# Performance work log

Measured on AMD Instinct MI355X. Metric: run time of the kernel, lower is better.

The kernel has to match this reference:

```python
import jax, jax.numpy as jnp
import numpy as np
from jax import lax

K = 5  # carafe kernel size


def conv2d(x, w, b=None, padding='SAME'):
    y = lax.conv_general_dilated(x, w, (1, 1), padding,
                                 dimension_numbers=('NHWC', 'HWIO', 'NHWC'))
    return y if b is None else y + b


def upsample2x(x):
    return jnp.repeat(jnp.repeat(x, 2, axis=1), 2, axis=2)


def carafe(coarse, kernel):
    # coarse: [B,H,W,C]; kernel: [B,2H,2W,K*K] predicted at fine resolution
    B, H, W, C = coarse.shape
    pad = K // 2
    p = jnp.pad(coarse, ((0, 0), (pad, pad), (pad, pad), (0, 0)))
    # [B,H,W,K*K,C] neighborhoods, row-major (di,dj) order
    patches = jnp.stack([p[:, di:di + H, dj:dj + W, :]
                         for di in range(K) for dj in range(K)], axis=3)
    # softmax-normalized reassembly weights; fine pixel (i,j) -> coarse (i//2,j//2)
    mask = jax.nn.softmax(kernel, axis=-1).reshape(B, H, 2, W, 2, K * K)
    out = jnp.einsum('bhxwyk,bhwkc->bhxwyc', mask, patches)
    return out.reshape(B, 2 * H, 2 * W, C)


def setup_inputs() -> dict:
    key = jax.random.key(0)
    ks = jax.random.split(key, 8)
    B, H, W = 4, 64, 64
    Cf, Cc, E, F = 128, 256, 64, 256
    s = lambda k, shape: jax.random.normal(k, shape, jnp.float32) * 0.05
    z = lambda n: jnp.zeros((n,), jnp.float32)
    return dict(
        fine=jax.random.normal(ks[0], (B, 2 * H, 2 * W, Cf), jnp.float32),
        coarse=jax.random.normal(ks[1], (B, H, W, Cc), jnp.float32),
        gate_w=s(ks[2], (1, 1, Cc, 1)), gate_b=z(1),
        ss_fine_w=s(ks[3], (1, 1, Cf, E)), ss_fine_b=z(E),
        ss_coarse_w=s(ks[4], (1, 1, Cc, E)),
        ss_content_w=s(ks[5], (3, 3, E, K * K)), ss_content_b=z(K * K),
        coarse_proj_w=s(ks[6], (1, 1, Cc, F)), coarse_proj_b=z(F),
        fine_proj_w=s(ks[7], (1, 1, F, F)), fine_proj_b=z(F),
    )


def reference(fine, coarse, gate_w, gate_b, ss_fine_w, ss_fine_b, ss_coarse_w,
              ss_content_w, ss_content_b, coarse_proj_w, coarse_proj_b,
              fine_proj_w, fine_proj_b):
    # gate branch: 1x1 conv + sigmoid on coarse, nearest-upsample to fine size
    gate = upsample2x(jax.nn.sigmoid(conv2d(coarse, gate_w, gate_b)))
    # SemiShift kernel prediction: shared 3x3 'content' conv on both embeddings
    f = conv2d(conv2d(fine, ss_fine_w, ss_fine_b), ss_content_w, ss_content_b)
    c = conv2d(conv2d(coarse, ss_coarse_w), ss_content_w, ss_content_b)
    kernel = f + upsample2x(c)  # [B,2H,2W,K*K]
    # CARAFE content-aware reassembly of coarse at fine resolution
    cu = carafe(coarse, kernel)
    c_out = conv2d(cu, coarse_proj_w, coarse_proj_b)
    # NOTE: faithful to source -- 'fine' projection is applied to the coarse output
    f_out = conv2d(c_out, fine_proj_w, fine_proj_b)
    return gate * f_out + (1.0 - gate) * c_out
```

## Files before the change

### kernel.cpp

```cpp
#include <hip/hip_runtime.h>
#include <math.h>

constexpr int Bb = 4, Hc = 64, Wc = 64, Cc = 256, Cf = 128, E = 64, KK = 25, F = 256;
constexpr int Hf = 128, Wf = 128;
constexpr int Nc = Bb * Hc * Wc;
constexpr int Nf = Bb * Hf * Wf;

typedef __attribute__((ext_vector_type(8))) short bf16x8;
typedef __attribute__((ext_vector_type(4))) float f32x4;

__device__ inline unsigned short f2b(float f) {
  union { float f; unsigned u; } v; v.f = f;
  return (unsigned short)((v.u + 0x7FFF + ((v.u >> 16) & 1)) >> 16);
}

__global__ __launch_bounds__(256) void prepA_kernel(
    const float* __restrict__ fw, const float* __restrict__ cw,
    const float* __restrict__ cntw, unsigned short* __restrict__ Wtf,
    unsigned short* __restrict__ Wtc, unsigned short* __restrict__ Wtcnt) {
  int gid = blockIdx.x * 256 + threadIdx.x;
  if (gid < 8192) {
    int i = gid;
    int n = i & 63, k = i >> 6;
    Wtf[n * 128 + k] = f2b(fw[i]);
  } else if (gid < 8192 + 16384) {
    int i = gid - 8192;
    int n = i & 63, k = i >> 6;
    Wtc[n * 256 + k] = f2b(cw[i]);
  } else if (gid < 8192 + 16384 + 18432) {
    int i = gid - 8192 - 16384;
    int n = i & 31, kk = i >> 5;
    Wtcnt[n * 576 + kk] = (n < 25) ? f2b(cntw[kk * 25 + n]) : (unsigned short)0;
  }
}

template <int K>
__device__ inline void emb_body(const float* __restrict__ in,
                                const unsigned short* __restrict__ Wt,
                                const float* __restrict__ bias,
                                unsigned short* __restrict__ out, int pxb,
                                unsigned short* a_s ) {
  constexpr int LDA = 136;
  int t = threadIdx.x;
  int wid = t >> 6, lane = t & 63;
  int lr = lane & 15, lg = lane >> 4;
  const f32x4 zero4 = {0.f, 0.f, 0.f, 0.f};
  f32x4 acc[4] = {zero4, zero4, zero4, zero4};

  #pragma unroll
  for (int c0 = 0; c0 < K; c0 += 128) {
    for (int idx = t; idx < 64 * 32; idx += 256) {
      int px = idx >> 5, kc = idx & 31;
      float4 v = *(const float4*)&in[(size_t)(pxb + px) * K + c0 + kc * 4];
      *(short4*)&a_s[px * LDA + kc * 4] =
          make_short4((short)f2b(v.x), (short)f2b(v.y), (short)f2b(v.z), (short)f2b(v.w));
    }
    __syncthreads();
    #pragma unroll
    for (int kt = 0; kt < 4; kt++) {
      bf16x8 a = *(const bf16x8*)&a_s[(wid * 16 + lr) * LDA + kt * 32 + lg * 8];
      #pragma unroll
      for (int nt = 0; nt < 4; nt++) {
        bf16x8 bb = *(const bf16x8*)&Wt[(size_t)(nt * 16 + lr) * K + c0 + kt * 32 + lg * 8];
        acc[nt] = __builtin_amdgcn_mfma_f32_16x16x32_bf16(a, bb, acc[nt], 0, 0, 0);
      }
    }
    if (c0 + 128 < K) __syncthreads();
  }

  #pragma unroll
  for (int nt = 0; nt < 4; nt++) {
    int n = nt * 16 + lr;
    float bv = bias ? bias[n] : 0.f;
    #pragma unroll
    for (int r = 0; r < 4; r++) {
      int px = wid * 16 + lg * 4 + r;
      out[(size_t)(pxb + px) * 64 + n] = f2b(acc[nt][r] + bv);
    }
  }
}

__global__ __launch_bounds__(256) void emb_both_kernel(
    const float* __restrict__ fine, const unsigned short* __restrict__ Wtf,
    const float* __restrict__ fbias, unsigned short* __restrict__ femb,
    const float* __restrict__ coarse, const unsigned short* __restrict__ Wtc,
    unsigned short* __restrict__ cemb) {
  __shared__ __align__(16) unsigned short a_s[64 * 136];
  int idx = blockIdx.x;
  if (idx < Nf / 64) emb_body<128>(fine, Wtf, fbias, femb, idx * 64, a_s);
  else               emb_body<256>(coarse, Wtc, nullptr, cemb, (idx - Nf / 64) * 64, a_s);
}

__global__ __launch_bounds__(256) void content_fused_kernel(
    const unsigned short* __restrict__ femb, const unsigned short* __restrict__ cemb,
    const unsigned short* __restrict__ Wtcnt, const float* __restrict__ cb,
    float* __restrict__ kff, float* __restrict__ kfc,
    const float* __restrict__ coarse, const float* __restrict__ gw,
    const float* __restrict__ gb, float* __restrict__ gatec,
    const float* __restrict__ W1, const float* __restrict__ W2,
    unsigned short* __restrict__ Wt1, unsigned short* __restrict__ Wt12,
    float* __restrict__ b12f, const float* __restrict__ b1,
    const float* __restrict__ b2) {
  __shared__ __align__(16) unsigned short a_s[324 * 72];
  int idx = blockIdx.x, t = threadIdx.x;

  if (idx < 256) {
    int w = t >> 6, lane = t & 63;
    int base = idx * 64 + w * 16;
    const float4 wv = *(const float4*)(gw + lane * 4);
    float gb0 = gb[0];
    #pragma unroll
    for (int rnd = 0; rnd < 2; rnd++) {
      int p0 = base + rnd * 8;
      float a0, a1, a2, a3, a4, a5, a6, a7;
      {
        float4 v0 = *(const float4*)(coarse + (size_t)(p0 + 0) * 256 + lane * 4);
        float4 v1 = *(const float4*)(coarse + (size_t)(p0 + 1) * 256 + lane * 4);
        float4 v2 = *(const float4*)(coarse + (size_t)(p0 + 2) * 256 + lane * 4);
        float4 v3 = *(const float4*)(coarse + (size_t)(p0 + 3) * 256 + lane * 4);
        float4 v4 = *(const float4*)(coarse + (size_t)(p0 + 4) * 256 + lane * 4);
        float4 v5 = *(const float4*)(coarse + (size_t)(p0 + 5) * 256 + lane * 4);
        float4 v6 = *(const float4*)(coarse + (size_t)(p0 + 6) * 256 + lane * 4);
        float4 v7 = *(const float4*)(coarse + (size_t)(p0 + 7) * 256 + lane * 4);
        a0 = v0.x * wv.x + v0.y * wv.y + v0.z * wv.z + v0.w * wv.w;
        a1 = v1.x * wv.x + v1.y * wv.y + v1.z * wv.z + v1.w * wv.w;
        a2 = v2.x * wv.x + v2.y * wv.y + v2.z * wv.z + v2.w * wv.w;
        a3 = v3.x * wv.x + v3.y * wv.y + v3.z * wv.z + v3.w * wv.w;
        a4 = v4.x * wv.x + v4.y * wv.y + v4.z * wv.z + v4.w * wv.w;
        a5 = v5.x * wv.x + v5.y * wv.y + v5.z * wv.z + v5.w * wv.w;
        a6 = v6.x * wv.x + v6.y * wv.y + v6.z * wv.z + v6.w * wv.w;
        a7 = v7.x * wv.x + v7.y * wv.y + v7.z * wv.z + v7.w * wv.w;
      }
      #pragma unroll
      for (int off2 = 32; off2; off2 >>= 1) {
        a0 += __shfl_xor(a0, off2);
        a1 += __shfl_xor(a1, off2);
        a2 += __shfl_xor(a2, off2);
        a3 += __shfl_xor(a3, off2);
        a4 += __shfl_xor(a4, off2);
        a5 += __shfl_xor(a5, off2);
        a6 += __shfl_xor(a6, off2);
        a7 += __shfl_xor(a7, off2);
      }
      if (lane == 0) {
        gatec[p0 + 0] = 1.f / (1.f + expf(-(a0 + gb0)));
        gatec[p0 + 1] = 1.f / (1.f + expf(-(a1 + gb0)));
        gatec[p0 + 2] = 1.f / (1.f + expf(-(a2 + gb0)));
        gatec[p0 + 3] = 1.f / (1.f + expf(-(a3 + gb0)));
        gatec[p0 + 4] = 1.f / (1.f + expf(-(a4 + gb0)));
        gatec[p0 + 5] = 1.f / (1.f + expf(-(a5 + gb0)));
        gatec[p0 + 6] = 1.f / (1.f + expf(-(a6 + gb0)));
        gatec[p0 + 7] = 1.f / (1.f + expf(-(a7 + gb0)));
      }
    }
    return;
  } else if (idx < 272) {
    float (*tile)[65] = (float(*)[65])a_s;
    int sub = idx - 256;
    int k0 = ((sub >> 2) & 3) * 64, n0 = (sub & 3) * 64;
    int r0 = t >> 6, c = t & 63;
    #pragma unroll
    for (int r = r0; r < 64; r += 4)
      tile[r][c] = W1[(size_t)(k0 + r) * 256 + n0 + c];
    __syncthreads();
    #pragma unroll
    for (int r = r0; r < 64; r += 4)
      Wt1[(size_t)(n0 + r) * 256 + k0 + c] = f2b(tile[c][r]);
    return;
  } else if (idx < 288) {
    unsigned short* aa = a_s;
    unsigned short* bs = a_s + 64 * 72;
    int sub = idx - 272;
    int nbase = (sub & 3) * 64, k0 = (sub >> 2) * 64;
    int wid = t >> 6, lane = t & 63;
    int lr = lane & 15, lg = lane >> 4;
    const f32x4 zero4 = {0.f, 0.f, 0.f, 0.f};
    f32x4 acc[4] = {zero4, zero4, zero4, zero4};

    for (int mc = 0; mc < 4; mc++) {
      for (int i = t; i < 64 * 16; i += 256) {
        int r = i >> 4, c4 = i & 15;
        float4 v = *(const float4*)&W1[(size_t)(k0 + r) * 256 + mc * 64 + c4 * 4];
        *(short4*)&aa[r * 72 + c4 * 4] =
            make_short4((short)f2b(v.x), (short)f2b(v.y), (short)f2b(v.z), (short)f2b(v.w));
      }
      for (int i = t; i < 64 * 16; i += 256) {
        int m = i >> 4, n4 = i & 15;
        float4 v = *(const float4*)&W2[(size_t)(mc * 64 + m) * 256 + nbase + n4 * 4];
        bs[(n4 * 4 + 0) * 72 + m] = f2b(v.x);
        bs[(n4 * 4 + 1) * 72 + m] = f2b(v.y);
        bs[(n4 * 4 + 2) * 72 + m] = f2b(v.z);
        bs[(n4 * 4 + 3) * 72 + m] = f2b(v.w);
      }
      __syncthreads();
      #pragma unroll
      for (int kt = 0; kt < 2; kt++) {
        bf16x8 a = *(const bf16x8*)&aa[(wid * 16 + lr) * 72 + kt * 32 + lg * 8];
        #pragma unroll
        for (int nt = 0; nt < 4; nt++) {
          bf16x8 bb = *(const bf16x8*)&bs[(nt * 16 + lr) * 72 + kt * 32 + lg * 8];
          acc[nt] = __builtin_amdgcn_mfma_f32_16x16x32_bf16(a, bb, acc[nt], 0, 0, 0);
        }
      }
      __syncthreads();
    }
    #pragma unroll
    for (int nt = 0; nt < 4; nt++)
      #pragma unroll
      for (int r = 0; r < 4; r++)
        Wt12[(size_t)(nbase + nt * 16 + lr) * 256 + k0 + wid * 16 + lg * 4 + r] =
            f2b(acc[nt][r]);
    return;
  } else if (idx == 288) {
    int n = t;
    float a0 = 0.f, a1 = 0.f, a2 = 0.f, a3 = 0.f;
    #pragma unroll 4
    for (int m = 0; m < 256; m += 4) {
      a0 += b1[m + 0] * W2[(size_t)(m + 0) * 256 + n];
      a1 += b1[m + 1] * W2[(size_t)(m + 1) * 256 + n];
      a2 += b1[m + 2] * W2[(size_t)(m + 2) * 256 + n];
      a3 += b1[m + 3] * W2[(size_t)(m + 3) * 256 + n];
    }
    b12f[n] = (a0 + a1) + (a2 + a3) + b2[n];
    return;
  }

  int cidx = idx - 289;
  const unsigned short* emb;
  float* out;
  int b, i0, j0, Hd, Wd;
  if (cidx < 256) {
    b = cidx >> 6; int rem = cidx & 63;
    i0 = (rem >> 3) * 16; j0 = (rem & 7) * 16; Hd = 128; Wd = 128;
    emb = femb; out = kff;
  } else {
    int i2 = cidx - 256;
    b = i2 >> 4; int rem = i2 & 15;
    i0 = (rem >> 2) * 16; j0 = (rem & 3) * 16; Hd = 64; Wd = 64;
    emb = cemb; out = kfc;
  }

  for (int i = t; i < 324 * 16; i += 256) {
    int cell = i >> 4, ck = i & 15;
    int gi = i0 - 1 + cell / 18;
    int gj = j0 - 1 + cell % 18;
    short4 v = make_short4(0, 0, 0, 0);
    if (gi >= 0 && gi < Hd && gj >= 0 && gj < Wd)
      v = *(const short4*)&emb[(size_t)((b * Hd + gi) * Wd + gj) * 64 + ck * 4];
    *(short4*)&a_s[cell * 72 + ck * 4] = v;
  }
  __syncthreads();

  int wid = t >> 6, lane = t & 63;
  int lr = lane & 15, lg = lane >> 4;
  const f32x4 zero4 = {0.f, 0.f, 0.f, 0.f};
  f32x4 acc[4][2];
  #pragma unroll
  for (int mt = 0; mt < 4; mt++)
    #pragma unroll
    for (int nt = 0; nt < 2; nt++) acc[mt][nt] = zero4;

  #pragma unroll
  for (int nt = 0; nt < 2; nt++) {
    bf16x8 wb[9][2];
    #pragma unroll
    for (int tap = 0; tap < 9; tap++)
      #pragma unroll
      for (int kt = 0; kt < 2; kt++)
        wb[tap][kt] = *(const bf16x8*)&Wtcnt[(size_t)(nt * 16 + lr) * 576 + tap * 64 + kt * 32 + lg * 8];

    #pragma unroll
    for (int mt = 0; mt < 4; mt++) {
      int m = wid * 4 + mt;
      #pragma unroll
      for (int di = 0; di < 3; di++) {
        #pragma unroll
        for (int dj = 0; dj < 3; dj++) {
          int cell = (m + di) * 18 + (lr + dj);
          int tap = di * 3 + dj;
          #pragma unroll
          for (int kt = 0; kt < 2; kt++) {
            bf16x8 a = *(const bf16x8*)&a_s[cell * 72 + kt * 32 + lg * 8];
            acc[mt][nt] = __builtin_amdgcn_mfma_f32_16x16x32_bf16(a, wb[tap][kt], acc[mt][nt], 0, 0, 0);
          }
        }
      }
    }
  }

  #pragma unroll
  for (int mt = 0; mt < 4; mt++) {
    int m = wid * 4 + mt;
    int gi = i0 + m;
    #pragma unroll
    for (int nt = 0; nt < 2; nt++) {
      int ch = nt * 16 + lr;
      if (ch < 25) {
        float bv = cb[ch];
        #pragma unroll
        for (int r = 0; r < 4; r++) {
          int gj = j0 + lg * 4 + r;
          out[(size_t)((b * Hd + gi) * Wd + gj) * 25 + ch] = acc[mt][nt][r] + bv;
        }
      }
    }
  }
}

__global__ __launch_bounds__(256) void carafe_kernel(
    const float* __restrict__ coarse, const float* __restrict__ kff,
    const float* __restrict__ kfc, unsigned short* __restrict__ cu_g) {
  __shared__ __align__(16) unsigned short buf[256 * 72];
  __shared__ __align__(16) unsigned short m_ext[64 * 72];
  unsigned short* win_t = buf;
  unsigned short* cu_s  = buf;

  int t = threadIdx.x;
  int b = blockIdx.z;
  int i0 = blockIdx.y * 8, j0 = blockIdx.x * 8;
  int hw0 = (i0 >> 1) - 2, ww0 = (j0 >> 1) - 2;

  {
    #pragma unroll
    for (int p0 = 0; p0 < 64; p0 += 4) {
      unsigned short vals[4];
      #pragma unroll
      for (int q = 0; q < 4; q++) {
        int p = p0 + q;
        int h = hw0 + (p >> 3), w = ww0 + (p & 7);
        float v = 0.f;
        if (h >= 0 && h < 64 && w >= 0 && w < 64)
          v = coarse[(size_t)((b * 64 + h) * 64 + w) * 256 + t];
        vals[q] = f2b(v);
      }
      *(short4*)&win_t[t * 72 + p0] =
          make_short4((short)vals[0], (short)vals[1], (short)vals[2], (short)vals[3]);
    }
  }
  if (t < 64) {
    int ti = t >> 3, tj = t & 7;
    int i = i0 + ti, j = j0 + tj;
    size_t fpx = (size_t)((b * 128 + i) * 128 + j);
    size_t cpx = (size_t)((b * 64 + (i >> 1)) * 64 + (j >> 1));
    float v[25];
    float mx = -1e30f;
    #pragma unroll
    for (int m = 0; m < 25; m++) {
      v[m] = kff[fpx * 25 + m] + kfc[cpx * 25 + m];
      mx = fmaxf(mx, v[m]);
    }
    float s = 0.f;
    #pragma unroll
    for (int m = 0; m < 25; m++) { v[m] = expf(v[m] - mx); s += v[m]; }
    float inv = 1.f / s;
    unsigned* row32 = (unsigned*)&m_ext[t * 72];
    #pragma unroll
    for (int q = 0; q < 36; q++) row32[q] = 0;
    int wib = ti >> 1, wjb = tj >> 1;
    #pragma unroll
    for (int di = 0; di < 5; di++)
      #pragma unroll
      for (int dj = 0; dj < 5; dj++)
        m_ext[t * 72 + (wib + di) * 8 + (wjb + dj)] = f2b(v[di * 5 + dj] * inv);
  }
  __syncthreads();

  int wid = t >> 6, lane = t & 63;
  int lr = lane & 15, lg = lane >> 4;
  const f32x4 zero4 = {0.f, 0.f, 0.f, 0.f};

  f32x4 acc0[4][4];
  #pragma unroll
  for (int mi = 0; mi < 4; mi++)
    #pragma unroll
    for (int ni = 0; ni < 4; ni++) acc0[mi][ni] = zero4;
  #pragma unroll
  for (int kt = 0; kt < 2; kt++) {
    bf16x8 am[4];
    #pragma unroll
    for (int mi = 0; mi < 4; mi++)
      am[mi] = *(const bf16x8*)&m_ext[(mi * 16 + lr) * 72 + kt * 32 + lg * 8];
    #pragma unroll
    for (int ni = 0; ni < 4; ni++) {
      bf16x8 bb = *(const bf16x8*)&win_t[(size_t)(wid * 64 + ni * 16 + lr) * 72 + kt * 32 + lg * 8];
      #pragma unroll
      for (int mi = 0; mi < 4; mi++)
        acc0[mi][ni] = __builtin_amdgcn_mfma_f32_16x16x32_bf16(am[mi], bb, acc0[mi][ni], 0, 0, 0);
    }
  }
  __syncthreads();

  #pragma unroll
  for (int mi = 0; mi < 4; mi++)
    #pragma unroll
    for (int ni = 0; ni < 4; ni++)
      #pragma unroll
      for (int r = 0; r < 4; r++)
        cu_s[(mi * 16 + lg * 4 + r) * 264 + wid * 64 + ni * 16 + lr] = f2b(acc0[mi][ni][r]);
  __syncthreads();

  for (int c = t; c < 2048; c += 256) {
    int p = c >> 5, off = (c & 31) << 3;
    int gi = i0 + (p >> 3), gj = j0 + (p & 7);
    bf16x8 v = *(const bf16x8*)&cu_s[p * 264 + off];
    *(bf16x8*)&cu_g[(size_t)((b * 128 + gi) * 128 + gj) * 256 + off] = v;
  }
}

__global__ __launch_bounds__(256, 2) void proj_kernel(
    const unsigned short* __restrict__ cu_g, const float* __restrict__ gatec,
    const unsigned short* __restrict__ Wt1, const float* __restrict__ b1,
    const unsigned short* __restrict__ Wt12, const float* __restrict__ b12,
    float* __restrict__ out) {
  __shared__ __align__(16) unsigned short a_s[2][64 * 264];
  __shared__ float g_s[2][32];
  int t = threadIdx.x;
  int bid = blockIdx.x;
  int cg = bid >> 8;
  int g  = bid & 255;
  int wid = t >> 6, lane = t & 63;
  int lr = lane & 15, lg = lane >> 4;
  int n0 = cg * 64 + wid * 16;

  bf16x8 wb1[8], wb12[8];
  #pragma unroll
  for (int kt = 0; kt < 8; kt++) {
    size_t wrow = (size_t)(n0 + lr) * 256 + kt * 32 + lg * 8;
    wb1[kt]  = *(const bf16x8*)&Wt1[wrow];
    wb12[kt] = *(const bf16x8*)&Wt12[wrow];
  }
  float b1v  = b1[n0 + lr];
  float b12v = b12[n0 + lr];

  {
    size_t m0 = (size_t)g * 256;
    for (int c = t; c < 2048; c += 256) {
      int row = c >> 5, off = (c & 31) << 3;
      *(bf16x8*)&a_s[0][row * 264 + off] = *(const bf16x8*)&cu_g[(m0 + row) * 256 + off];
    }
    if (t < 32) {
      int b_ = (int)(m0 >> 14), ii = (int)((m0 >> 7) & 127), j0 = (int)(m0 & 127);
      g_s[0][t] = gatec[(size_t)(b_ * 64 + (ii >> 1)) * 64 + (j0 >> 1) + t];
    }
  }
  __syncthreads();

  const f32x4 zero4 = {0.f, 0.f, 0.f, 0.f};

  for (int it = 0; it < 4; ++it) {
    int cur = it & 1, nxt = cur ^ 1;
    size_t m0i = (size_t)(g * 4 + it) * 64;

    bf16x8 pf[8];
    float gpf = 0.f;
    if (it < 3) {
      size_t m0n = m0i + 64;
      #pragma unroll
      for (int q = 0; q < 8; q++) {
        int c = t + q * 256;
        int row = c >> 5, off = (c & 31) << 3;
        pf[q] = *(const bf16x8*)&cu_g[(m0n + row) * 256 + off];
      }
      if (t < 32) {
        int b_ = (int)(m0n >> 14), ii = (int)((m0n >> 7) & 127), j0 = (int)(m0n & 127);
        gpf = gatec[(size_t)(b_ * 64 + (ii >> 1)) * 64 + (j0 >> 1) + t];
      }
    }

    f32x4 accc[4] = {zero4, zero4, zero4, zero4};
    f32x4 accf[4] = {zero4, zero4, zero4, zero4};
    #pragma unroll
    for (int kt = 0; kt < 8; kt++) {
      #pragma unroll
      for (int mi = 0; mi < 4; mi++) {
        bf16x8 a = *(const bf16x8*)&a_s[cur][(mi * 16 + lr) * 264 + kt * 32 + lg * 8];
        accc[mi] = __builtin_amdgcn_mfma_f32_16x16x32_bf16(a, wb1[kt],  accc[mi], 0, 0, 0);
        accf[mi] = __builtin_amdgcn_mfma_f32_16x16x32_bf16(a, wb12[kt], accf[mi], 0, 0, 0);
      }
    }

    if (it < 3) {
      #pragma unroll
      for (int q = 0; q < 8; q++) {
        int c = t + q * 256;
        int row = c >> 5, off = (c & 31) << 3;
        *(bf16x8*)&a_s[nxt][row * 264 + off] = pf[q];
      }
      if (t < 32) g_s[nxt][t] = gpf;
    }

    #pragma unroll
    for (int mi = 0; mi < 4; mi++) {
      #pragma unroll
      for (int r = 0; r < 4; r++) {
        int row = mi * 16 + lg * 4 + r;
        float gg = g_s[cur][row >> 1];
        float f_out = accf[mi][r] + b12v;
        float c_out = accc[mi][r] + b1v;
        out[(m0i + row) * 256 + n0 + lr] = gg * f_out + (1.f - gg) * c_out;
      }
    }

    if (it < 3) __syncthreads();
  }
}

extern "C" void kernel_launch(void* const* d_in, const int* in_sizes, int n_in,
                              void* d_out, int out_size, void* d_ws, size_t ws_size,
                              hipStream_t stream) {
  const float* fine        = (const float*)d_in[0];
  const float* coarse      = (const float*)d_in[1];
  const float* gate_w      = (const float*)d_in[2];
  const float* gate_b      = (const float*)d_in[3];
  const float* ss_fine_w   = (const float*)d_in[4];
  const float* ss_fine_b   = (const float*)d_in[5];
  const float* ss_coarse_w = (const float*)d_in[6];
  const float* ss_content_w= (const float*)d_in[7];
  const float* ss_content_b= (const float*)d_in[8];
  const float* W1          = (const float*)d_in[9];
  const float* b1          = (const float*)d_in[10];
  const float* W2          = (const float*)d_in[11];
  const float* b2          = (const float*)d_in[12];
  float* out = (float*)d_out;

  char* ws = (char*)d_ws;
  size_t off = 0;
  float* gatec = (float*)(ws + off); off += 131072;
  unsigned short* femb = (unsigned short*)(ws + off); off += (size_t)Nf * 64 * 2;
  unsigned short* cemb = (unsigned short*)(ws + off); off += (size_t)Nc * 64 * 2;
  float* kff   = (float*)(ws + off); off += (size_t)Nf * 25 * 4;
  float* kfc   = (float*)(ws + off); off += (size_t)Nc * 25 * 4;
  unsigned short* Wt1 = (unsigned short*)(ws + off); off += 65536 * 2;
  unsigned short* Wtf = (unsigned short*)(ws + off); off += 64 * 128 * 2;
  unsigned short* Wtc = (unsigned short*)(ws + off); off += 64 * 256 * 2;
  unsigned short* Wtcnt = (unsigned short*)(ws + off); off += 32 * 576 * 2;
  unsigned short* Wt12 = (unsigned short*)(ws + off); off += 65536 * 2;
  float* b12f = (float*)(ws + off); off += 1024;
  unsigned short* cu_g = (unsigned short*)(ws + off); off += (size_t)Nf * 256 * 2;

  prepA_kernel<<<168, 256, 0, stream>>>(ss_fine_w, ss_coarse_w, ss_content_w,
                                        Wtf, Wtc, Wtcnt);
  emb_both_kernel<<<Nf / 64 + Nc / 64, 256, 0, stream>>>(
      fine, Wtf, ss_fine_b, femb, coarse, Wtc, cemb);
  content_fused_kernel<<<289 + 256 + 64, 256, 0, stream>>>(
      femb, cemb, Wtcnt, ss_content_b, kff, kfc,
      coarse, gate_w, gate_b, gatec, W1, W2, Wt1, Wt12, b12f, b1, b2);
  carafe_kernel<<<dim3(Wf / 8, Hf / 8, Bb), 256, 0, stream>>>(coarse, kff, kfc, cu_g);
  proj_kernel<<<1024, 256, 0, stream>>>(cu_g, gatec, Wt1, b1, Wt12, b12f, out);
}
```

Baseline: 114.4 us.

## Pipeline embedding GEMM with double-buffered LDS and persistent multi-tile blocks

The embedding 1x1-conv kernel now has each block process four 64-pixel tiles, 320 blocks instead of 1280. Global loads for the next 128-channel chunk are prefetched into registers while MFMAs run on the current chunk, with two LDS buffers alternating. This aims to hide global-load latency and cut launch and sync overhead. It doubles LDS use and raises register pressure, and with only 320 blocks there is less parallelism across CUs.

After: 115.6 us. No clear change (+1.1%).

```diff
diff --git a/kernel.cpp b/kernel.cpp
--- a/kernel.cpp
+++ b/kernel.cpp
@@ -34,61 +34,94 @@
   }
 }
 
-template <int K>
-__device__ inline void emb_body(const float* __restrict__ in,
+template <int K, int UNITS>
+__device__ inline void emb_pipe(const float* __restrict__ in,
                                 const unsigned short* __restrict__ Wt,
                                 const float* __restrict__ bias,
-                                unsigned short* __restrict__ out, int pxb,
-                                unsigned short* a_s ) {
+                                unsigned short* __restrict__ out,
+                                int tile0, unsigned short* a_s ) {
   constexpr int LDA = 136;
+  constexpr int CPT = K / 128;
   int t = threadIdx.x;
   int wid = t >> 6, lane = t & 63;
   int lr = lane & 15, lg = lane >> 4;
+  int px_s = t >> 5;
+  int kc_s = t & 31;
   const f32x4 zero4 = {0.f, 0.f, 0.f, 0.f};
   f32x4 acc[4] = {zero4, zero4, zero4, zero4};
 
-  #pragma unroll
-  for (int c0 = 0; c0 < K; c0 += 128) {
-    for (int idx = t; idx < 64 * 32; idx += 256) {
-      int px = idx >> 5, kc = idx & 31;
-      float4 v = *(const float4*)&in[(size_t)(pxb + px) * K + c0 + kc * 4];
-      *(short4*)&a_s[px * LDA + kc * 4] =
-          make_short4((short)f2b(v.x), (short)f2b(v.y), (short)f2b(v.z), (short)f2b(v.w));
-    }
-    __syncthreads();
+  {
+    const float* src = in + (size_t)tile0 * 64 * K;
+    float4 pf[8];
+    #pragma unroll
+    for (int q = 0; q < 8; q++)
+      pf[q] = *(const float4*)&src[(size_t)(px_s + q * 8) * K + kc_s * 4];
+    #pragma unroll
+    for (int q = 0; q < 8; q++)
+      *(short4*)&a_s[(px_s + q * 8) * LDA + kc_s * 4] =
+          make_short4((short)f2b(pf[q].x), (short)f2b(pf[q].y),
+                      (short)f2b(pf[q].z), (short)f2b(pf[q].w));
+  }
+  __syncthreads();
+
+  for (int u = 0; u < UNITS; ++u) {
+    int cur = u & 1, nxt = cur ^ 1;
+
+    float4 nf[8];
+    if (u + 1 < UNITS) {
+      int tile = tile0 + (u + 1) / CPT, ch = ((u + 1) % CPT) * 128;
+      const float* src = in + (size_t)tile * 64 * K + ch;
+      #pragma unroll
+      for (int q = 0; q < 8; q++)
+        nf[q] = *(const float4*)&src[(size_t)(px_s + q * 8) * K + kc_s * 4];
+    }
+
+    int ch = (u % CPT) * 128;
     #pragma unroll
     for (int kt = 0; kt < 4; kt++) {
-      bf16x8 a = *(const bf16x8*)&a_s[(wid * 16 + lr) * LDA + kt * 32 + lg * 8];
+      bf16x8 a = *(const bf16x8*)&a_s[cur * 64 * LDA + (wid * 16 + lr) * LDA + kt * 32 + lg * 8];
       #pragma unroll
       for (int nt = 0; nt < 4; nt++) {
-        bf16x8 bb = *(const bf16x8*)&Wt[(size_t)(nt * 16 + lr) * K + c0 + kt * 32 + lg * 8];
+        bf16x8 bb = *(const bf16x8*)&Wt[(size_t)(nt * 16 + lr) * K + ch + kt * 32 + lg * 8];
         acc[nt] = __builtin_amdgcn_mfma_f32_16x16x32_bf16(a, bb, acc[nt], 0, 0, 0);
       }
     }
-    if (c0 + 128 < K) __syncthreads();
-  }
-
-  #pragma unroll
-  for (int nt = 0; nt < 4; nt++) {
-    int n = nt * 16 + lr;
-    float bv = bias ? bias[n] : 0.f;
-    #pragma unroll
-    for (int r = 0; r < 4; r++) {
-      int px = wid * 16 + lg * 4 + r;
-      out[(size_t)(pxb + px) * 64 + n] = f2b(acc[nt][r] + bv);
-    }
-  }
-}
-
-__global__ __launch_bounds__(256) void emb_both_kernel(
+
+    if ((u % CPT) == CPT - 1) {
+      int pxb = (tile0 + u / CPT) * 64;
+      #pragma unroll
+      for (int nt = 0; nt < 4; nt++) {
+        int n = nt * 16 + lr;
+        float bv = bias ? bias[n] : 0.f;
+        #pragma unroll
+        for (int r = 0; r < 4; r++) {
+          int px = wid * 16 + lg * 4 + r;
+          out[(size_t)(pxb + px) * 64 + n] = f2b(acc[nt][r] + bv);
+        }
+        acc[nt] = zero4;
+      }
+    }
+
+    if (u + 1 < UNITS) {
+      #pragma unroll
+      for (int q = 0; q < 8; q++)
+        *(short4*)&a_s[nxt * 64 * LDA + (px_s + q * 8) * LDA + kc_s * 4] =
+            make_short4((short)f2b(nf[q].x), (short)f2b(nf[q].y),
+                        (short)f2b(nf[q].z), (short)f2b(nf[q].w));
+      __syncthreads();
+    }
+  }
+}
+
+__global__ __launch_bounds__(256) void emb_pipe_kernel(
     const float* __restrict__ fine, const unsigned short* __restrict__ Wtf,
     const float* __restrict__ fbias, unsigned short* __restrict__ femb,
     const float* __restrict__ coarse, const unsigned short* __restrict__ Wtc,
     unsigned short* __restrict__ cemb) {
-  __shared__ __align__(16) unsigned short a_s[64 * 136];
+  __shared__ __align__(16) unsigned short a_s[2 * 64 * 136];
   int idx = blockIdx.x;
-  if (idx < Nf / 64) emb_body<128>(fine, Wtf, fbias, femb, idx * 64, a_s);
-  else               emb_body<256>(coarse, Wtc, nullptr, cemb, (idx - Nf / 64) * 64, a_s);
+  if (idx < 256) emb_pipe<128, 4>(fine, Wtf, fbias, femb, idx * 4, a_s);
+  else           emb_pipe<256, 8>(coarse, Wtc, nullptr, cemb, (idx - 256) * 4, a_s);
 }
 
 __global__ __launch_bounds__(256) void content_fused_kernel(
@@ -540,7 +573,7 @@
 
   prepA_kernel<<<168, 256, 0, stream>>>(ss_fine_w, ss_coarse_w, ss_content_w,
                                         Wtf, Wtc, Wtcnt);
-  emb_both_kernel<<<Nf / 64 + Nc / 64, 256, 0, stream>>>(
+  emb_pipe_kernel<<<320, 256, 0, stream>>>(
       fine, Wtf, ss_fine_b, femb, coarse, Wtc, cemb);
   content_fused_kernel<<<289 + 256 + 64, 256, 0, stream>>>(
       femb, cemb, Wtcnt, ss_content_b, kff, kfc,
```
